# Performance work log

Measured on AMD Instinct MI355X. Metric: run time of the kernel, lower is better.

## Reference

```python
import jax, jax.numpy as jnp
import numpy as np

HEADS = 8
EPS = 1e-6
LN_EPS = 1e-5


def avg_pool(x, k):
    b, c, h, w = x.shape
    return x.reshape(b, c, h // k, k, w // k, k).mean(axis=(3, 5))


def layernorm(x, g, b):
    mu = x.mean(-1, keepdims=True)
    var = x.var(-1, keepdims=True)
    return (x - mu) / jnp.sqrt(var + LN_EPS) * g + b


def pos_embed_2d(h, w, c):
    # original calls build_2d_sincos_position_embedding(w=h, h=w): grid over (h, w), row-major flatten
    gw, gh = jnp.meshgrid(jnp.arange(h, dtype=jnp.float32),
                          jnp.arange(w, dtype=jnp.float32), indexing='ij')
    pd = c // 4
    omega = 1.0 / (10000.0 ** (jnp.arange(pd, dtype=jnp.float32) / pd))
    ow = gw.reshape(-1, 1) * omega  # (h*w, pd)
    oh = gh.reshape(-1, 1) * omega
    return jnp.concatenate([jnp.sin(ow), jnp.cos(ow), jnp.sin(oh), jnp.cos(oh)], axis=1)  # (h*w, c)


def _forward(a3, a4, q_w, q_b, q_ln_g, q_ln_b, k_w, k_b, k_ln_g, k_ln_b,
             v_w, v_b, out_w, out_b, lin1_w, lin1_b, lin2_w, lin2_b,
             n1_g, n1_b, n2_g, n2_b, idx):
    orig_a3 = a3
    if idx == 2:
        a3d = avg_pool(a3, 2)
    else:
        a3d = avg_pool(a3, 4)
        a4 = avg_pool(a4, 2)
    bs, c, h, w = a3d.shape
    L = h * w  # tgt_len == src_len (a3_down and a4 have equal spatial size)
    hd = c // HEADS

    residual = a3d.reshape(bs, c, L).transpose(0, 2, 1)  # (b, L, c)
    x3 = residual
    x4 = a4.reshape(bs, c, L).transpose(0, 2, 1)
    pos = pos_embed_2d(h, w, c)  # (L, c)
    x3 = x3 + pos[None]
    x4 = x4 + pos[None]

    Q = layernorm(x3 @ q_w + q_b, q_ln_g, q_ln_b)
    K = layernorm(x4 @ k_w + k_b, k_ln_g, k_ln_b)
    V = x4 @ v_w + v_b
    Q = jax.nn.relu(Q).reshape(bs, L, HEADS, hd).transpose(0, 2, 1, 3)  # (b,h,L,d)
    K = jax.nn.relu(K).reshape(bs, L, HEADS, hd).transpose(0, 2, 1, 3)
    V = V.reshape(bs, L, HEADS, hd).transpose(0, 2, 1, 3)

    # cosFormer position reweighting: index = pi/2 * (1..m) / m
    m = L
    wi = (np.pi / 2.0) * jnp.arange(1, m + 1, dtype=jnp.float32) / m  # (m,)
    sn = jnp.sin(wi)[None, None, :, None]
    cs = jnp.cos(wi)[None, None, :, None]
    Q_ = jnp.concatenate([Q * sn, Q * cs], axis=-1)  # (b,h,L,2d)
    K_ = jnp.concatenate([K * sn, K * cs], axis=-1)

    KV = jnp.einsum('bhld,bhlm->bhdm', K_, V)                     # (b,h,2d,d)
    Z = 1.0 / jnp.maximum(jnp.einsum('bhld,bhd->bhl', Q_, K_.sum(axis=2)), EPS)
    attn = jnp.einsum('bhld,bhdm->bhlm', Q_, KV) * Z[..., None]   # (b,h,L,d)
    attn = attn.transpose(0, 2, 1, 3).reshape(bs, L, c)

    out = attn @ out_w + out_b
    out = layernorm(out, n1_g, n1_b)     # normalize_before=False -> norm1 applied
    out = residual + out                 # dropout=0
    res2 = out
    out = jax.nn.gelu(out @ lin1_w + lin1_b, approximate=False) @ lin2_w + lin2_b
    out = layernorm(out, n2_g, n2_b)
    out = res2 + out

    a3sa = out.transpose(0, 2, 1).reshape(bs, c, h, w)
    a3sa = jax.image.resize(a3sa, orig_a3.shape, method='bilinear')  # align_corners=False
    return a3sa * orig_a3


def setup_inputs() -> dict:
    key = jax.random.key(0)
    ks = jax.random.split(key, 10)
    B, C = 16, 256
    C4 = 4 * C

    def w(k, shp):
        return jax.random.normal(k, shp, dtype=jnp.float32) * 0.02

    return {
        'a3': jax.random.normal(ks[0], (B, C, 128, 128), dtype=jnp.float32),
        'a4': jax.random.normal(ks[1], (B, C, 64, 64), dtype=jnp.float32),
        'q_w': w(ks[2], (C, C)), 'q_b': jnp.zeros((C,), jnp.float32),
        'q_ln_g': jnp.ones((C,), jnp.float32), 'q_ln_b': jnp.zeros((C,), jnp.float32),
        'k_w': w(ks[3], (C, C)), 'k_b': jnp.zeros((C,), jnp.float32),
        'k_ln_g': jnp.ones((C,), jnp.float32), 'k_ln_b': jnp.zeros((C,), jnp.float32),
        'v_w': w(ks[4], (C, C)), 'v_b': jnp.zeros((C,), jnp.float32),
        'out_w': w(ks[5], (C, C)), 'out_b': jnp.zeros((C,), jnp.float32),
        'lin1_w': w(ks[6], (C, C4)), 'lin1_b': jnp.zeros((C4,), jnp.float32),
        'lin2_w': w(ks[7], (C4, C)), 'lin2_b': jnp.zeros((C,), jnp.float32),
        'n1_g': jnp.ones((C,), jnp.float32), 'n1_b': jnp.zeros((C,), jnp.float32),
        'n2_g': jnp.ones((C,), jnp.float32), 'n2_b': jnp.zeros((C,), jnp.float32),
        'idx': 2,
    }


def reference(a3, a4, q_w, q_b, q_ln_g, q_ln_b, k_w, k_b, k_ln_g, k_ln_b,
              v_w, v_b, out_w, out_b, lin1_w, lin1_b, lin2_w, lin2_b,
              n1_g, n1_b, n2_g, n2_b, idx):
    return _forward(a3, a4, q_w, q_b, q_ln_g, q_ln_b, k_w, k_b, k_ln_g, k_ln_b,
                    v_w, v_b, out_w, out_b, lin1_w, lin1_b, lin2_w, lin2_b,
                    n1_g, n1_b, n2_g, n2_b, idx)
```

## Files before the change

kernel.cpp:

```cpp
#include <hip/hip_runtime.h>
#include <hip/hip_bf16.h>
#include <math.h>

#define HEADS 8
#define LL 4096
#define CDIM 256
#define BATCH 16
#define NROWS (BATCH*LL)

typedef __attribute__((ext_vector_type(8))) __bf16 bf16x8;
typedef __attribute__((ext_vector_type(4))) __bf16 bf16x4;
typedef __attribute__((ext_vector_type(4))) float f32x4;

__device__ inline float b2f(ushort u) {
    union { unsigned u; float f; } v; v.u = ((unsigned)u) << 16; return v.f;
}
__device__ inline ushort f2b(float f) {
    union { float f; unsigned u; } v; v.f = f;
    unsigned r = (v.u + 0x7FFF + ((v.u >> 16) & 1)) >> 16;
    return (ushort)r;
}
__device__ inline void gload16(const void* g, void* l) {
    __builtin_amdgcn_global_load_lds(
        (const __attribute__((address_space(1))) unsigned int*)g,
        (__attribute__((address_space(3))) unsigned int*)l, 16, 0, 0);
}
__device__ inline float fast_gelu(float v) {
    float u = 0.7978845608028654f * v * (1.0f + 0.044715f * v * v);
    float e = exp2f(u * 2.885390081777927f);
    float t = 1.0f - 2.0f / (e + 1.0f);
    return 0.5f * v * (1.0f + t);
}

__global__ __launch_bounds__(256) void prep_kernel(
    float* __restrict__ pos, float* __restrict__ snc,
    const float* __restrict__ q_w, const float* __restrict__ k_w,
    const float* __restrict__ v_w, const float* __restrict__ o_w,
    const float* __restrict__ w1, const float* __restrict__ w2,
    ushort* __restrict__ wqT, ushort* __restrict__ wkT,
    ushort* __restrict__ wvT, ushort* __restrict__ woT,
    ushort* __restrict__ w1T, ushort* __restrict__ w2T,
    float* __restrict__ ksglob)
{
    __shared__ float t[32][33];
    int bid = blockIdx.x;
    int tid = threadIdx.x;
    if (bid == 1792) {
        for (int i = tid; i < BATCH * 2 * 256; i += 256) ksglob[i] = 0.0f;
        return;
    }
    if (bid < 1024) {
        int c = tid;
        int k = c & 63;
        float omega = expf(-(float)k * (9.210340371976184f / 64.0f));
        #pragma unroll
        for (int i = 0; i < 4; ++i) {
            int l = bid * 4 + i;
            int y = l >> 6, x = l & 63;
            float coord = (c < 128) ? (float)y : (float)x;
            float ang = coord * omega;
            float val = ((c & 127) < 64) ? sinf(ang) : cosf(ang);
            pos[l * CDIM + c] = val;
            if (c < 2) {
                float wi = 1.5707963267948966f * (float)(l + 1) / (float)LL;
                snc[l * 2 + c] = (c == 0) ? sinf(wi) : cosf(wi);
            }
        }
        return;
    }
    int id = bid - 1024;
    const float* W; ushort* Wt; int K, N, kb, nb;
    if (id < 64)       { W = q_w; Wt = wqT; K = 256;  N = 256;  kb = (id & 7) * 32;  nb = (id >> 3) * 32; }
    else if (id < 128) { id -= 64;  W = k_w; Wt = wkT; K = 256;  N = 256;  kb = (id & 7) * 32;  nb = (id >> 3) * 32; }
    else if (id < 192) { id -= 128; W = v_w; Wt = wvT; K = 256;  N = 256;  kb = (id & 7) * 32;  nb = (id >> 3) * 32; }
    else if (id < 256) { id -= 192; W = o_w; Wt = woT; K = 256;  N = 256;  kb = (id & 7) * 32;  nb = (id >> 3) * 32; }
    else if (id < 512) { id -= 256; W = w1;  Wt = w1T; K = 256;  N = 1024; kb = (id & 7) * 32;  nb = (id >> 3) * 32; }
    else               { id -= 512; W = w2;  Wt = w2T; K = 1024; N = 256;  kb = (id & 31) * 32; nb = (id >> 5) * 32; }
    int x = tid & 31, y = tid >> 5;
    #pragma unroll
    for (int i = 0; i < 4; ++i)
        t[y + i * 8][x] = W[(size_t)(kb + y + i * 8) * N + nb + x];
    __syncthreads();
    #pragma unroll
    for (int i = 0; i < 4; ++i) {
        int n = y + i * 8;
        Wt[(size_t)(nb + n) * K + kb + x] = f2b(t[x][n]);
    }
}

__global__ __launch_bounds__(256) void pool_x4_kernel(
    const float* __restrict__ a3, const float* __restrict__ a4,
    ushort* __restrict__ residual, ushort* __restrict__ x3b,
    ushort* __restrict__ x4b, const float* __restrict__ pos)
{
    __shared__ float raw[64][128];
    __shared__ float pooled[64][65];
    int tid = threadIdx.x;
    int ct = blockIdx.y;
    if (blockIdx.z < 16) {
        int i = blockIdx.x, b = blockIdx.z;
        #pragma unroll
        for (int it = 0; it < 8; ++it) {
            int lin = (it * 256 + tid) * 4;
            int x = lin & 127;
            int cc = lin >> 7;
            size_t base = ((size_t)(b * 256 + ct * 64 + cc) * 128 + 2 * i) * 128 + x;
            float4 v0 = *(const float4*)&a3[base];
            float4 v1 = *(const float4*)&a3[base + 128];
            float4 s = make_float4(v0.x + v1.x, v0.y + v1.y, v0.z + v1.z, v0.w + v1.w);
            *(float4*)&raw[cc][x] = s;
        }
        __syncthreads();
        #pragma unroll
        for (int it = 0; it < 16; ++it) {
            int idx = it * 256 + tid;
            int j = idx & 63, cc = idx >> 6;
            pooled[cc][j] = 0.25f * (raw[cc][2 * j] + raw[cc][2 * j + 1]);
        }
        __syncthreads();
        #pragma unroll
        for (int it = 0; it < 16; ++it) {
            int cc = tid & 63;
            int jj = (tid >> 6) + it * 4;
            float val = pooled[cc][jj];
            int l = i * 64 + jj;
            int c = ct * 64 + cc;
            size_t o = (size_t)(b * LL + l) * CDIM + c;
            residual[o] = f2b(val);
            x3b[o] = f2b(val + pos[l * CDIM + c]);
        }
    } else {
        int y = blockIdx.x, b = blockIdx.z - 16;
        #pragma unroll
        for (int it = 0; it < 16; ++it) {
            int idx = it * 256 + tid;
            int x = idx & 63, cc = idx >> 6;
            pooled[cc][x] = a4[((size_t)(b * 256 + ct * 64 + cc) * 64 + y) * 64 + x];
        }
        __syncthreads();
        #pragma unroll
        for (int it = 0; it < 16; ++it) {
            int cc = tid & 63;
            int xx = (tid >> 6) + it * 4;
            int l = y * 64 + xx, c = ct * 64 + cc;
            x4b[(size_t)(b * LL + l) * CDIM + c] = f2b(pooled[cc][xx] + pos[l * CDIM + c]);
        }
    }
}

template<bool DO_LN, bool DO_RELU, bool DO_RES>
__global__ __launch_bounds__(512, 4) void gemm_mfma(
    const ushort* __restrict__ A, const ushort* __restrict__ Wt,
    const float* __restrict__ bias, const float* __restrict__ gam_,
    const float* __restrict__ bet_, const ushort* __restrict__ res,
    ushort* __restrict__ outb)
{
    __shared__ ushort As[2][128 * 32];
    __shared__ ushort Bs[2][256 * 32];
    __shared__ float redS[128][4];
    __shared__ float redQ[128][4];
    __shared__ float2 mustd[128];

    const int tid = threadIdx.x;
    const int lane = tid & 63;
    const int wv = tid >> 6;
    const int wr = wv >> 2;
    const int wc = wv & 3;
    const int wvu = __builtin_amdgcn_readfirstlane(wv);
    const int row0 = blockIdx.x * 128;

    const int sr = tid >> 2;
    const int sg = (tid & 3) ^ ((sr >> 1) & 3);
    const ushort* aSrc = A + (size_t)(row0 + sr) * 256 + sg * 8;
    const ushort* bSrc0 = Wt + (size_t)sr * 256 + sg * 8;
    const ushort* bSrc1 = Wt + (size_t)(128 + sr) * 256 + sg * 8;

    const int frSlot = (lane >> 4) ^ (((lane & 15) >> 1) & 3);

    f32x4 acc[4][4] = {};
    gload16(aSrc, (char*)&As[0][0] + wvu * 1024);
    gload16(bSrc0, (char*)&Bs[0][0] + wvu * 1024);
    gload16(bSrc1, (char*)&Bs[0][0] + 8192 + wvu * 1024);
    __syncthreads();

    int cur = 0;
    for (int t = 0; t < 8; ++t) {
        if (t < 7) {
            gload16(aSrc + (t + 1) * 32, (char*)&As[cur ^ 1][0] + wvu * 1024);
            gload16(bSrc0 + (t + 1) * 32, (char*)&Bs[cur ^ 1][0] + wvu * 1024);
            gload16(bSrc1 + (t + 1) * 32, (char*)&Bs[cur ^ 1][0] + 8192 + wvu * 1024);
        }
        bf16x8 af[4], bfr[4];
        #pragma unroll
        for (int f = 0; f < 4; ++f) {
            int r = wr * 64 + f * 16 + (lane & 15);
            af[f] = *(const bf16x8*)&As[cur][r * 32 + frSlot * 8];
            int c = wc * 64 + f * 16 + (lane & 15);
            bfr[f] = *(const bf16x8*)&Bs[cur][c * 32 + frSlot * 8];
        }
        __builtin_amdgcn_s_setprio(1);
        #pragma unroll
        for (int fi = 0; fi < 4; ++fi)
            #pragma unroll
            for (int fj = 0; fj < 4; ++fj)
                acc[fi][fj] = __builtin_amdgcn_mfma_f32_16x16x32_bf16(
                    af[fi], bfr[fj], acc[fi][fj], 0, 0, 0);
        __builtin_amdgcn_s_setprio(0);
        __syncthreads();
        cur ^= 1;
    }

    const int cl = lane & 15;
    const int rg = lane >> 4;
    float bia[4], gmv[4], btv[4];
    #pragma unroll
    for (int fj = 0; fj < 4; ++fj) {
        int col = wc * 64 + fj * 16 + cl;
        bia[fj] = bias[col];
        if constexpr (DO_LN) { gmv[fj] = gam_[col]; btv[fj] = bet_[col]; }
    }
    #pragma unroll
    for (int fi = 0; fi < 4; ++fi)
        #pragma unroll
        for (int fj = 0; fj < 4; ++fj)
            #pragma unroll
            for (int j = 0; j < 4; ++j)
                acc[fi][fj][j] += bia[fj];

    if constexpr (DO_LN) {
        #pragma unroll
        for (int fi = 0; fi < 4; ++fi)
            #pragma unroll
            for (int j = 0; j < 4; ++j) {
                float s = acc[fi][0][j] + acc[fi][1][j] + acc[fi][2][j] + acc[fi][3][j];
                float q = acc[fi][0][j] * acc[fi][0][j] + acc[fi][1][j] * acc[fi][1][j]
                        + acc[fi][2][j] * acc[fi][2][j] + acc[fi][3][j] * acc[fi][3][j];
                #pragma unroll
                for (int m = 1; m <= 8; m <<= 1) {
                    s += __shfl_xor(s, m, 64);
                    q += __shfl_xor(q, m, 64);
                }
                if (cl == 0) {
                    int tr = wr * 64 + fi * 16 + rg * 4 + j;
                    redS[tr][wc] = s; redQ[tr][wc] = q;
                }
            }
        __syncthreads();
        if (tid < 128) {
            float s = redS[tid][0] + redS[tid][1] + redS[tid][2] + redS[tid][3];
            float q = redQ[tid][0] + redQ[tid][1] + redQ[tid][2] + redQ[tid][3];
            float mu = s * (1.0f / 256.0f);
            float var = q * (1.0f / 256.0f) - mu * mu;
            mustd[tid] = make_float2(mu, rsqrtf(var + 1e-5f));
        }
        __syncthreads();
        #pragma unroll
        for (int fi = 0; fi < 4; ++fi)
            #pragma unroll
            for (int j = 0; j < 4; ++j) {
                float2 ms = mustd[wr * 64 + fi * 16 + rg * 4 + j];
                #pragma unroll
                for (int fj = 0; fj < 4; ++fj)
                    acc[fi][fj][j] = (acc[fi][fj][j] - ms.x) * ms.y * gmv[fj] + btv[fj];
            }
    }
    if constexpr (DO_RELU) {
        #pragma unroll
        for (int fi = 0; fi < 4; ++fi)
            #pragma unroll
            for (int fj = 0; fj < 4; ++fj)
                #pragma unroll
                for (int j = 0; j < 4; ++j)
                    acc[fi][fj][j] = fmaxf(acc[fi][fj][j], 0.0f);
    }
    #pragma unroll
    for (int fi = 0; fi < 4; ++fi)
        #pragma unroll
        for (int j = 0; j < 4; ++j) {
            size_t row = row0 + wr * 64 + fi * 16 + rg * 4 + j;
            size_t rbase = row * 256 + wc * 64 + cl;
            #pragma unroll
            for (int fj = 0; fj < 4; ++fj) {
                float v = acc[fi][fj][j];
                if constexpr (DO_RES) v += b2f(res[rbase + fj * 16]);
                outb[rbase + fj * 16] = f2b(v);
            }
        }
}

__global__ __launch_bounds__(512, 2) void gemm_kv(
    const ushort* __restrict__ A, const ushort* __restrict__ wkT,
    const ushort* __restrict__ wvT, const float* __restrict__ k_b,
    const float* __restrict__ k_g, const float* __restrict__ k_beta,
    const float* __restrict__ v_b, const float* __restrict__ snc,
    float* __restrict__ ksglob, ushort* __restrict__ Kb, ushort* __restrict__ Vb)
{
    __shared__ ushort As[2][128 * 32];
    __shared__ ushort BsK[2][256 * 32];
    __shared__ ushort BsV[2][256 * 32];
    float*  redS  = (float*)&As[0][0];
    float*  redQ  = redS + 512;
    float2* mustd = (float2*)(redQ + 512);

    const int tid = threadIdx.x;
    const int lane = tid & 63;
    const int wv = tid >> 6;
    const int wr = wv >> 2;
    const int wc = wv & 3;
    const int wvu = __builtin_amdgcn_readfirstlane(wv);
    const int row0 = blockIdx.x * 128;

    const int sr = tid >> 2;
    const int sg = (tid & 3) ^ ((sr >> 1) & 3);
    const ushort* aSrc = A + (size_t)(row0 + sr) * 256 + sg * 8;
    const ushort* bkSrc0 = wkT + (size_t)sr * 256 + sg * 8;
    const ushort* bkSrc1 = wkT + (size_t)(128 + sr) * 256 + sg * 8;
    const ushort* bvSrc0 = wvT + (size_t)sr * 256 + sg * 8;
    const ushort* bvSrc1 = wvT + (size_t)(128 + sr) * 256 + sg * 8;

    const int frSlot = (lane >> 4) ^ (((lane & 15) >> 1) & 3);

    f32x4 accK[4][4] = {};
    f32x4 accV[4][4] = {};
    gload16(aSrc, (char*)&As[0][0] + wvu * 1024);
    gload16(bkSrc0, (char*)&BsK[0][0] + wvu * 1024);
    gload16(bkSrc1, (char*)&BsK[0][0] + 8192 + wvu * 1024);
    gload16(bvSrc0, (char*)&BsV[0][0] + wvu * 1024);
    gload16(bvSrc1, (char*)&BsV[0][0] + 8192 + wvu * 1024);
    __syncthreads();

    int cur = 0;
    for (int t = 0; t < 8; ++t) {
        if (t < 7) {
            gload16(aSrc + (t + 1) * 32, (char*)&As[cur ^ 1][0] + wvu * 1024);
            gload16(bkSrc0 + (t + 1) * 32, (char*)&BsK[cur ^ 1][0] + wvu * 1024);
            gload16(bkSrc1 + (t + 1) * 32, (char*)&BsK[cur ^ 1][0] + 8192 + wvu * 1024);
            gload16(bvSrc0 + (t + 1) * 32, (char*)&BsV[cur ^ 1][0] + wvu * 1024);
            gload16(bvSrc1 + (t + 1) * 32, (char*)&BsV[cur ^ 1][0] + 8192 + wvu * 1024);
        }
        bf16x8 af[4], bk[4], bv[4];
        #pragma unroll
        for (int f = 0; f < 4; ++f) {
            int r = wr * 64 + f * 16 + (lane & 15);
            af[f] = *(const bf16x8*)&As[cur][r * 32 + frSlot * 8];
            int c = wc * 64 + f * 16 + (lane & 15);
            bk[f] = *(const bf16x8*)&BsK[cur][c * 32 + frSlot * 8];
            bv[f] = *(const bf16x8*)&BsV[cur][c * 32 + frSlot * 8];
        }
        __builtin_amdgcn_s_setprio(1);
        #pragma unroll
        for (int fi = 0; fi < 4; ++fi)
            #pragma unroll
            for (int fj = 0; fj < 4; ++fj) {
                accK[fi][fj] = __builtin_amdgcn_mfma_f32_16x16x32_bf16(
                    af[fi], bk[fj], accK[fi][fj], 0, 0, 0);
                accV[fi][fj] = __builtin_amdgcn_mfma_f32_16x16x32_bf16(
                    af[fi], bv[fj], accV[fi][fj], 0, 0, 0);
            }
        __builtin_amdgcn_s_setprio(0);
        __syncthreads();
        cur ^= 1;
    }

    const int cl = lane & 15;
    const int rg = lane >> 4;
    #pragma unroll
    for (int fj = 0; fj < 4; ++fj) {
        float bv_ = v_b[wc * 64 + fj * 16 + cl];
        #pragma unroll
        for (int fi = 0; fi < 4; ++fi)
            #pragma unroll
            for (int j = 0; j < 4; ++j)
                accV[fi][fj][j] += bv_;
    }
    #pragma unroll
    for (int fi = 0; fi < 4; ++fi)
        #pragma unroll
        for (int j = 0; j < 4; ++j) {
            size_t rbase = (size_t)(row0 + wr * 64 + fi * 16 + rg * 4 + j) * 256 + wc * 64 + cl;
            #pragma unroll
            for (int fj = 0; fj < 4; ++fj)
                Vb[rbase + fj * 16] = f2b(accV[fi][fj][j]);
        }
    float bia[4], gmv[4], btv[4];
    #pragma unroll
    for (int fj = 0; fj < 4; ++fj) {
        int col = wc * 64 + fj * 16 + cl;
        bia[fj] = k_b[col]; gmv[fj] = k_g[col]; btv[fj] = k_beta[col];
    }
    #pragma unroll
    for (int fi = 0; fi < 4; ++fi)
        #pragma unroll
        for (int fj = 0; fj < 4; ++fj)
            #pragma unroll
            for (int j = 0; j < 4; ++j)
                accK[fi][fj][j] += bia[fj];
    #pragma unroll
    for (int fi = 0; fi < 4; ++fi)
        #pragma unroll
        for (int j = 0; j < 4; ++j) {
            float s = accK[fi][0][j] + accK[fi][1][j] + accK[fi][2][j] + accK[fi][3][j];
            float q = accK[fi][0][j] * accK[fi][0][j] + accK[fi][1][j] * accK[fi][1][j]
                    + accK[fi][2][j] * accK[fi][2][j] + accK[fi][3][j] * accK[fi][3][j];
            #pragma unroll
            for (int m = 1; m <= 8; m <<= 1) {
                s += __shfl_xor(s, m, 64);
                q += __shfl_xor(q, m, 64);
            }
            if (cl == 0) {
                int tr = wr * 64 + fi * 16 + rg * 4 + j;
                redS[tr * 4 + wc] = s; redQ[tr * 4 + wc] = q;
            }
        }
    __syncthreads();
    if (tid < 128) {
        float s = redS[tid * 4] + redS[tid * 4 + 1] + redS[tid * 4 + 2] + redS[tid * 4 + 3];
        float q = redQ[tid * 4] + redQ[tid * 4 + 1] + redQ[tid * 4 + 2] + redQ[tid * 4 + 3];
        float mu = s * (1.0f / 256.0f);
        float var = q * (1.0f / 256.0f) - mu * mu;
        mustd[tid] = make_float2(mu, rsqrtf(var + 1e-5f));
    }
    __syncthreads();
    float kss[4] = {}, ksc[4] = {};
    #pragma unroll
    for (int fi = 0; fi < 4; ++fi)
        #pragma unroll
        for (int j = 0; j < 4; ++j) {
            int rloc = wr * 64 + fi * 16 + rg * 4 + j;
            float2 ms = mustd[rloc];
            int l = (row0 + rloc) & (LL - 1);
            float sn = snc[l * 2], cs = snc[l * 2 + 1];
            size_t rbase = (size_t)(row0 + rloc) * 256 + wc * 64 + cl;
            #pragma unroll
            for (int fj = 0; fj < 4; ++fj) {
                float v = (accK[fi][fj][j] - ms.x) * ms.y * gmv[fj] + btv[fj];
                v = fmaxf(v, 0.0f);
                Kb[rbase + fj * 16] = f2b(v);
                kss[fj] += sn * v;
                ksc[fj] += cs * v;
            }
        }
    int b = row0 >> 12;
    #pragma unroll
    for (int fj = 0; fj < 4; ++fj) {
        float s = kss[fj], c = ksc[fj];
        s += __shfl_xor(s, 16, 64); s += __shfl_xor(s, 32, 64);
        c += __shfl_xor(c, 16, 64); c += __shfl_xor(c, 32, 64);
        if (rg == 0) {
            int col = wc * 64 + fj * 16 + cl;
            atomicAdd(&ksglob[((size_t)b * 2 + 0) * 256 + col], s);
            atomicAdd(&ksglob[((size_t)b * 2 + 1) * 256 + col], c);
        }
    }
}

__global__ __launch_bounds__(256, 2) void mlp_fused(
    const ushort* __restrict__ res2, const ushort* __restrict__ w1T,
    const ushort* __restrict__ w2T, const float* __restrict__ b1,
    const float* __restrict__ b2, const float* __restrict__ gam_,
    const float* __restrict__ bet_, ushort* __restrict__ outb)
{
    __shared__ ushort As[2][64 * 32];
    __shared__ ushort Bs[2][256 * 32];
    __shared__ ushort h1c[8 * 64 * 36];
    __shared__ float redS[64][4];
    __shared__ float redQ[64][4];
    __shared__ float2 mustd[64];

    const int tid = threadIdx.x;
    const int lane = tid & 63;
    const int wv = tid >> 6;
    const int wvu = __builtin_amdgcn_readfirstlane(wv);
    const int row0 = blockIdx.x * 64;
    const int sr = tid >> 2;
    const int sg = (tid & 3) ^ ((sr >> 1) & 3);
    const ushort* aSrc = res2 + (size_t)(row0 + sr) * 256 + sg * 8;
    const int frSlot = (lane >> 4) ^ (((lane & 15) >> 1) & 3);
    const int cl = lane & 15;
    const int rg = lane >> 4;

    f32x4 acc2[4][4] = {};
    gload16(aSrc, (char*)&As[0][0] + wvu * 1024);
    #pragma unroll
    for (int j = 0; j < 4; ++j)
        gload16(w1T + (size_t)(j * 64 + sr) * 256 + sg * 8,
                (char*)&Bs[0][0] + j * 4096 + wvu * 1024);
    __syncthreads();
    int cur = 0;

    for (int c = 0; c < 4; ++c) {
        const ushort* b1Src = w1T + (size_t)(c * 256 + sr) * 256 + sg * 8;
        const ushort* b2Src = w2T + (size_t)sr * 1024 + c * 256 + sg * 8;
        f32x4 acc1[4][4] = {};
        for (int t = 0; t < 8; ++t) {
            if (t < 7) {
                gload16(aSrc + (t + 1) * 32, (char*)&As[cur ^ 1][0] + wvu * 1024);
                #pragma unroll
                for (int j = 0; j < 4; ++j)
                    gload16(b1Src + j * 64 * 256 + (t + 1) * 32,
                            (char*)&Bs[cur ^ 1][0] + j * 4096 + wvu * 1024);
            } else {
                gload16(aSrc, (char*)&As[cur ^ 1][0] + wvu * 1024);
                #pragma unroll
                for (int j = 0; j < 4; ++j)
                    gload16(b2Src + (size_t)j * 64 * 1024,
                            (char*)&Bs[cur ^ 1][0] + j * 4096 + wvu * 1024);
            }
            bf16x8 af[4], bfr[4];
            #pragma unroll
            for (int f = 0; f < 4; ++f) {
                int r = f * 16 + (lane & 15);
                af[f] = *(const bf16x8*)&As[cur][r * 32 + frSlot * 8];
                int cc2 = wv * 64 + f * 16 + (lane & 15);
                bfr[f] = *(const bf16x8*)&Bs[cur][cc2 * 32 + frSlot * 8];
            }
            __builtin_amdgcn_s_setprio(1);
            #pragma unroll
            for (int fi = 0; fi < 4; ++fi)
                #pragma unroll
                for (int fj = 0; fj < 4; ++fj)
                    acc1[fi][fj] = __builtin_amdgcn_mfma_f32_16x16x32_bf16(
                        af[fi], bfr[fj], acc1[fi][fj], 0, 0, 0);
            __builtin_amdgcn_s_setprio(0);
            __syncthreads();
            cur ^= 1;
        }
        float bia1[4];
        #pragma unroll
        for (int fj = 0; fj < 4; ++fj)
            bia1[fj] = b1[c * 256 + wv * 64 + fj * 16 + cl];
        #pragma unroll
        for (int fi = 0; fi < 4; ++fi)
            #pragma unroll
            for (int fj = 0; fj < 4; ++fj) {
                int tch = wv * 2 + (fj >> 1);
                int kk_local = (fj & 1) * 16 + cl;
                #pragma unroll
                for (int j = 0; j < 4; ++j) {
                    float v = acc1[fi][fj][j] + bia1[fj];
                    float g = fast_gelu(v);
                    int row = fi * 16 + rg * 4 + j;
                    h1c[tch * 2304 + row * 36 + kk_local] = f2b(g);
                }
            }
        __syncthreads();
        for (int t = 0; t < 8; ++t) {
            if (t < 7) {
                #pragma unroll
                for (int j = 0; j < 4; ++j)
                    gload16(b2Src + (size_t)j * 64 * 1024 + (t + 1) * 32,
                            (char*)&Bs[cur ^ 1][0] + j * 4096 + wvu * 1024);
            } else {
                int cn = (c < 3) ? c + 1 : 3;
                #pragma unroll
                for (int j = 0; j < 4; ++j)
                    gload16(w1T + (size_t)(cn * 256 + j * 64 + sr) * 256 + sg * 8,
                            (char*)&Bs[cur ^ 1][0] + j * 4096 + wvu * 1024);
            }
            bf16x8 af[4], bfr[4];
            #pragma unroll
            for (int f = 0; f < 4; ++f) {
                int r = f * 16 + (lane & 15);
                int ho = t * 2304 + r * 36 + (lane >> 4) * 8;
                bf16x4 lo = *(const bf16x4*)&h1c[ho];
                bf16x4 hi = *(const bf16x4*)&h1c[ho + 4];
                bf16x8 a_;
                a_[0] = lo[0]; a_[1] = lo[1]; a_[2] = lo[2]; a_[3] = lo[3];
                a_[4] = hi[0]; a_[5] = hi[1]; a_[6] = hi[2]; a_[7] = hi[3];
                af[f] = a_;
                int cc2 = wv * 64 + f * 16 + (lane & 15);
                bfr[f] = *(const bf16x8*)&Bs[cur][cc2 * 32 + frSlot * 8];
            }
            __builtin_amdgcn_s_setprio(1);
            #pragma unroll
            for (int fi = 0; fi < 4; ++fi)
                #pragma unroll
                for (int fj = 0; fj < 4; ++fj)
                    acc2[fi][fj] = __builtin_amdgcn_mfma_f32_16x16x32_bf16(
                        af[fi], bfr[fj], acc2[fi][fj], 0, 0, 0);
            __builtin_amdgcn_s_setprio(0);
            __syncthreads();
            cur ^= 1;
        }
    }
    float bia[4], gmv[4], btv[4];
    #pragma unroll
    for (int fj = 0; fj < 4; ++fj) {
        int col = wv * 64 + fj * 16 + cl;
        bia[fj] = b2[col];
        gmv[fj] = gam_[col];
        btv[fj] = bet_[col];
    }
    #pragma unroll
    for (int fi = 0; fi < 4; ++fi)
        #pragma unroll
        for (int fj = 0; fj < 4; ++fj)
            #pragma unroll
            for (int j = 0; j < 4; ++j)
                acc2[fi][fj][j] += bia[fj];
    #pragma unroll
    for (int fi = 0; fi < 4; ++fi)
        #pragma unroll
        for (int j = 0; j < 4; ++j) {
            float s = acc2[fi][0][j] + acc2[fi][1][j] + acc2[fi][2][j] + acc2[fi][3][j];
            float q = acc2[fi][0][j] * acc2[fi][0][j] + acc2[fi][1][j] * acc2[fi][1][j]
                    + acc2[fi][2][j] * acc2[fi][2][j] + acc2[fi][3][j] * acc2[fi][3][j];
            #pragma unroll
            for (int m = 1; m <= 8; m <<= 1) {
                s += __shfl_xor(s, m, 64);
                q += __shfl_xor(q, m, 64);
            }
            if (cl == 0) { redS[fi * 16 + rg * 4 + j][wv] = s; redQ[fi * 16 + rg * 4 + j][wv] = q; }
        }
    __syncthreads();
    if (tid < 64) {
        float s = redS[tid][0] + redS[tid][1] + redS[tid][2] + redS[tid][3];
        float q = redQ[tid][0] + redQ[tid][1] + redQ[tid][2] + redQ[tid][3];
        float mu = s * (1.0f / 256.0f);
        float var = q * (1.0f / 256.0f) - mu * mu;
        mustd[tid] = make_float2(mu, rsqrtf(var + 1e-5f));
    }
    __syncthreads();
    #pragma unroll
    for (int fi = 0; fi < 4; ++fi)
        #pragma unroll
        for (int j = 0; j < 4; ++j) {
            float2 ms = mustd[fi * 16 + rg * 4 + j];
            size_t row = row0 + fi * 16 + rg * 4 + j;
            size_t rbase = row * 256 + wv * 64 + cl;
            #pragma unroll
            for (int fj = 0; fj < 4; ++fj) {
                float v = (acc2[fi][fj][j] - ms.x) * ms.y * gmv[fj] + btv[fj];
                v += b2f(res2[rbase + fj * 16]);
                outb[rbase + fj * 16] = f2b(v);
            }
        }
}

__global__ __launch_bounds__(256) void kv_kernel(
    const ushort* __restrict__ Kmat, const ushort* __restrict__ Vmat,
    const float* __restrict__ snc, float* __restrict__ kvpart)
{
    __shared__ float Kt[64][36];
    __shared__ float Vt[64][36];
    __shared__ float sns[64], css[64];
    int chunk = blockIdx.x;
    int bh = blockIdx.y;
    int b = bh >> 3, h = bh & 7;
    int tid = threadIdx.x;
    int m = tid & 31;
    int d0 = (tid >> 5) * 4;
    float accs[4] = {}, accc[4] = {};
    int l0chunk = chunk * 512;
    int lrow = tid >> 2;
    int lcol = (tid & 3) * 8;
    for (int sub = 0; sub < 8; ++sub) {
        int l0 = l0chunk + sub * 64;
        {
            size_t gbase = (size_t)(b * LL + l0 + lrow) * CDIM + h * 32 + lcol;
            uint4 kr = *(const uint4*)&Kmat[gbase];
            uint4 vr = *(const uint4*)&Vmat[gbase];
            float* kd = &Kt[lrow][lcol];
            float* vd = &Vt[lrow][lcol];
            kd[0] = b2f((ushort)(kr.x & 0xffff)); kd[1] = b2f((ushort)(kr.x >> 16));
            kd[2] = b2f((ushort)(kr.y & 0xffff)); kd[3] = b2f((ushort)(kr.y >> 16));
            kd[4] = b2f((ushort)(kr.z & 0xffff)); kd[5] = b2f((ushort)(kr.z >> 16));
            kd[6] = b2f((ushort)(kr.w & 0xffff)); kd[7] = b2f((ushort)(kr.w >> 16));
            vd[0] = b2f((ushort)(vr.x & 0xffff)); vd[1] = b2f((ushort)(vr.x >> 16));
            vd[2] = b2f((ushort)(vr.y & 0xffff)); vd[3] = b2f((ushort)(vr.y >> 16));
            vd[4] = b2f((ushort)(vr.z & 0xffff)); vd[5] = b2f((ushort)(vr.z >> 16));
            vd[6] = b2f((ushort)(vr.w & 0xffff)); vd[7] = b2f((ushort)(vr.w >> 16));
        }
        if (tid < 64) { sns[tid] = snc[(l0 + tid) * 2]; css[tid] = snc[(l0 + tid) * 2 + 1]; }
        __syncthreads();
        #pragma unroll 4
        for (int lt = 0; lt < 64; ++lt) {
            float v = Vt[lt][m];
            float vs = v * sns[lt];
            float vc = v * css[lt];
            float4 kd4 = *(const float4*)&Kt[lt][d0];
            accs[0] += kd4.x * vs; accc[0] += kd4.x * vc;
            accs[1] += kd4.y * vs; accc[1] += kd4.y * vc;
            accs[2] += kd4.z * vs; accc[2] += kd4.z * vc;
            accs[3] += kd4.w * vs; accc[3] += kd4.w * vc;
        }
        __syncthreads();
    }
    size_t base = (size_t)(bh * 8 + chunk) * 2048;
    #pragma unroll
    for (int i2 = 0; i2 < 4; ++i2) {
        kvpart[base + (d0 + i2) * 32 + m] = accs[i2];
        kvpart[base + 1024 + (d0 + i2) * 32 + m] = accc[i2];
    }
}

__global__ __launch_bounds__(256) void kvred_kernel(
    const float* __restrict__ kvpart, const float* __restrict__ ksglob,
    ushort* __restrict__ Bimg)
{
    int bh = blockIdx.x;
    int b = bh >> 3, h = bh & 7;
    int tid = threadIdx.x;
    for (int e = tid; e < 2560; e += 256) {
        int n = e >> 5;
        int k = e & 31;
        int t = n >> 4, col = n & 15;
        float v = 0.0f;
        if (t < 4) {
            int off = (t >= 2 ? 1024 : 0) + k * 32 + (t & 1) * 16 + col;
            #pragma unroll
            for (int ch = 0; ch < 8; ++ch)
                v += kvpart[(size_t)(bh * 8 + ch) * 2048 + off];
        } else if (col < 2) {
            v = ksglob[((size_t)b * 2 + col) * 256 + h * 32 + k];
        }
        ushort hi = f2b(v);
        ushort lo = f2b(v - b2f(hi));
        Bimg[(size_t)bh * 5120 + n * 32 + k] = hi;
        Bimg[(size_t)bh * 5120 + (80 + n) * 32 + k] = lo;
    }
}

__global__ __launch_bounds__(256, 2) void attn_mfma(
    const ushort* __restrict__ Qmat, const ushort* __restrict__ Bimg,
    const float* __restrict__ snc, ushort* __restrict__ attnOut)
{
    __shared__ ushort Bs[5120];
    int ltile = blockIdx.x, h = blockIdx.y, b = blockIdx.z;
    int bh = b * 8 + h;
    int tid = threadIdx.x;
    int lane = tid & 63;
    int wv = tid >> 6;

    for (int e = tid; e < 640; e += 256)
        *(uint4*)&Bs[e * 8] = *(const uint4*)&Bimg[(size_t)bh * 5120 + e * 8];
    __syncthreads();

    bf16x8 bfr[10];
    #pragma unroll
    for (int tt = 0; tt < 10; ++tt) {
        int row = (tt < 5 ? tt * 16 : 80 + (tt - 5) * 16) + (lane & 15);
        bfr[tt] = *(const bf16x8*)&Bs[row * 32 + (lane >> 4) * 8];
    }
    int lbase = ltile * 256 + wv * 64;
    bf16x8 af[4];
    #pragma unroll
    for (int fi = 0; fi < 4; ++fi) {
        int l = lbase + fi * 16 + (lane & 15);
        af[fi] = *(const bf16x8*)&Qmat[(size_t)(b * LL + l) * CDIM + h * 32 + (lane >> 4) * 8];
    }
    f32x4 acc[4][5] = {};
    __builtin_amdgcn_s_setprio(1);
    #pragma unroll
    for (int fi = 0; fi < 4; ++fi)
        #pragma unroll
        for (int t = 0; t < 5; ++t) {
            acc[fi][t] = __builtin_amdgcn_mfma_f32_16x16x32_bf16(af[fi], bfr[t], acc[fi][t], 0, 0, 0);
            acc[fi][t] = __builtin_amdgcn_mfma_f32_16x16x32_bf16(af[fi], bfr[t + 5], acc[fi][t], 0, 0, 0);
        }
    __builtin_amdgcn_s_setprio(0);

    int zlane = lane & 48;
    int cl = lane & 15;
    #pragma unroll
    for (int fi = 0; fi < 4; ++fi) {
        #pragma unroll
        for (int j = 0; j < 4; ++j) {
            float zraw = acc[fi][4][j];
            float zs = __shfl(zraw, zlane, 64);
            float zc = __shfl(zraw, zlane | 1, 64);
            int l = lbase + fi * 16 + ((lane >> 4) & 3) * 4 + j;
            float sn = snc[l * 2], cs = snc[l * 2 + 1];
            float den = sn * zs + cs * zc;
            float Z = 1.0f / fmaxf(den, 1e-6f);
            float v0 = (sn * acc[fi][0][j] + cs * acc[fi][2][j]) * Z;
            float v1 = (sn * acc[fi][1][j] + cs * acc[fi][3][j]) * Z;
            size_t ob = (size_t)(b * LL + l) * CDIM + h * 32 + cl;
            attnOut[ob] = f2b(v0);
            attnOut[ob + 16] = f2b(v1);
        }
    }
}

__global__ __launch_bounds__(256) void resize_mul_kernel(
    const ushort* __restrict__ ffeat, const float* __restrict__ a3, float* __restrict__ out)
{
    __shared__ float ft[3][64][65];
    int k = blockIdx.x, ct = blockIdx.y, b = blockIdx.z;
    int tid = threadIdx.x;
    #pragma unroll
    for (int it = 0; it < 6; ++it) {
        int e = it * 256 + tid;
        int cg = e & 7;
        int xs = (e >> 3) & 63;
        int ys = e >> 9;
        int ysrc = min(max(k - 1 + ys, 0), 63);
        uint4 raw = *(const uint4*)&ffeat[(size_t)(b * LL + ysrc * 64 + xs) * CDIM + ct * 64 + cg * 8];
        float* dst = &ft[ys][cg * 8][xs];
        dst[0]   = b2f((ushort)(raw.x & 0xffff)); dst[65]  = b2f((ushort)(raw.x >> 16));
        dst[130] = b2f((ushort)(raw.y & 0xffff)); dst[195] = b2f((ushort)(raw.y >> 16));
        dst[260] = b2f((ushort)(raw.z & 0xffff)); dst[325] = b2f((ushort)(raw.z >> 16));
        dst[390] = b2f((ushort)(raw.w & 0xffff)); dst[455] = b2f((ushort)(raw.w >> 16));
    }
    __syncthreads();
    int x = tid & 127;
    int half = tid >> 7;
    int y = 2 * k + half;
    int ysA, ysB; float wyA, wyB;
    if (half == 0) { ysA = 0; ysB = 1; wyA = 0.25f; wyB = 0.75f; }
    else           { ysA = 1; ysB = 2; wyA = 0.75f; wyB = 0.25f; }
    int x0; float wx1;
    if ((x & 1) == 0) { x0 = x / 2 - 1; wx1 = 0.75f; }
    else              { x0 = x / 2;     wx1 = 0.25f; }
    int x0c = max(x0, 0);
    int x1c = min(x0 + 1, 63);
    float wx0 = 1.0f - wx1;
    for (int cc = 0; cc < 64; ++cc) {
        float rA = wx0 * ft[ysA][cc][x0c] + wx1 * ft[ysA][cc][x1c];
        float rB = wx0 * ft[ysB][cc][x0c] + wx1 * ft[ysB][cc][x1c];
        float val = wyA * rA + wyB * rB;
        size_t oidx = ((size_t)(b * 256 + ct * 64 + cc) * 128 + y) * 128 + x;
        out[oidx] = val * a3[oidx];
    }
}

extern "C" void kernel_launch(void* const* d_in, const int* in_sizes, int n_in,
                              void* d_out, int out_size, void* d_ws, size_t ws_size,
                              hipStream_t stream)
{
    const float* a3     = (const float*)d_in[0];
    const float* a4     = (const float*)d_in[1];
    const float* q_w    = (const float*)d_in[2];
    const float* q_b    = (const float*)d_in[3];
    const float* q_ln_g = (const float*)d_in[4];
    const float* q_ln_b = (const float*)d_in[5];
    const float* k_w    = (const float*)d_in[6];
    const float* k_b    = (const float*)d_in[7];
    const float* k_ln_g = (const float*)d_in[8];
    const float* k_ln_b = (const float*)d_in[9];
    const float* v_w    = (const float*)d_in[10];
    const float* v_b    = (const float*)d_in[11];
    const float* out_w  = (const float*)d_in[12];
    const float* out_b  = (const float*)d_in[13];
    const float* lin1_w = (const float*)d_in[14];
    const float* lin1_b = (const float*)d_in[15];
    const float* lin2_w = (const float*)d_in[16];
    const float* lin2_b = (const float*)d_in[17];
    const float* n1_g   = (const float*)d_in[18];
    const float* n1_b   = (const float*)d_in[19];
    const float* n2_g   = (const float*)d_in[20];
    const float* n2_b   = (const float*)d_in[21];
    float* out = (float*)d_out;
    char* base = (char*)d_ws;

    const size_t MiB = 1024 * 1024;
    float*  pos      = (float*)(base);
    float*  snc      = (float*)(base + 4 * MiB);
    ushort* wqT      = (ushort*)(base + 4 * MiB + 64 * 1024);
    ushort* wkT      = wqT + 256 * 256;
    ushort* wvT      = wkT + 256 * 256;
    ushort* woT      = wvT + 256 * 256;
    ushort* w1T      = woT + 256 * 256;
    ushort* w2T      = w1T + 1024 * 256;
    ushort* residual = (ushort*)(base + 6 * MiB);
    ushort* x3b      = (ushort*)(base + 38 * MiB);
    ushort* x4b      = (ushort*)(base + 70 * MiB);
    ushort* Qb       = (ushort*)(base + 102 * MiB);
    ushort* Kb       = (ushort*)(base + 134 * MiB);
    ushort* Vb       = (ushort*)(base + 166 * MiB);
    float*  kvp      = (float*)(base + 198 * MiB);
    float*  ksglob   = (float*)(base + 206 * MiB);
    ushort* Bimg     = (ushort*)(base + 207 * MiB);
    ushort* attnb    = x3b;
    ushort* res2b    = x4b;
    ushort* ffeat    = residual;

    prep_kernel<<<1793, 256, 0, stream>>>(pos, snc, q_w, k_w, v_w, out_w, lin1_w, lin2_w,
                                          wqT, wkT, wvT, woT, w1T, w2T, ksglob);
    pool_x4_kernel<<<dim3(64, 4, 32), 256, 0, stream>>>(a3, a4, residual, x3b, x4b, pos);

    gemm_mfma<true, true, false><<<NROWS / 128, 512, 0, stream>>>(
        x3b, wqT, q_b, q_ln_g, q_ln_b, nullptr, Qb);
    gemm_kv<<<NROWS / 128, 512, 0, stream>>>(
        x4b, wkT, wvT, k_b, k_ln_g, k_ln_b, v_b, snc, ksglob, Kb, Vb);

    kv_kernel<<<dim3(8, 128), 256, 0, stream>>>(Kb, Vb, snc, kvp);
    kvred_kernel<<<128, 256, 0, stream>>>(kvp, ksglob, Bimg);
    attn_mfma<<<dim3(16, 8, 16), 256, 0, stream>>>(Qb, Bimg, snc, attnb);

    gemm_mfma<true, false, true><<<NROWS / 128, 512, 0, stream>>>(
        attnb, woT, out_b, n1_g, n1_b, residual, res2b);
    mlp_fused<<<NROWS / 64, 256, 0, stream>>>(
        res2b, w1T, w2T, lin1_b, lin2_b, n2_g, n2_b, ffeat);

    resize_mul_kernel<<<dim3(64, 4, 16), 256, 0, stream>>>(ffeat, a3, out);
}
```

Measured before the change: 529.7 us.

## Merge prep and pooling kernels, fold kv reduction into attention kernel

Prep and pooling now run as a single kernel that computes the positional embedding inline instead of reading a precomputed table. Weight transposes and the snc/ksglob init move to extra grid slices, removing one launch and the 4 MiB pos buffer round trip. The kv reduction kernel is removed: each attention block reduces kvpart partials and builds its bf16 hi/lo B image directly in shared memory. The cost is redundant reduction work, repeated 16 times per (b,h) across l-tiles, plus extra transcendental math in the pooling path. Ordering is risky: gemm_kv accumulates into ksglob, which is now zeroed by one block of the same kernel that also transposes the weights, so correctness relies on the kernel boundary.

Measured after the change: 566.1 us. +6.9%, slower.

```diff
diff --git a/kernel.cpp b/kernel.cpp
--- a/kernel.cpp
+++ b/kernel.cpp
@@ -31,74 +31,35 @@
     float t = 1.0f - 2.0f / (e + 1.0f);
     return 0.5f * v * (1.0f + t);
 }
-
-__global__ __launch_bounds__(256) void prep_kernel(
-    float* __restrict__ pos, float* __restrict__ snc,
+__device__ inline float posval(int l, int c) {
+    int k = c & 63;
+    float omega = expf(-(float)k * (9.210340371976184f / 64.0f));
+    float coord = (c < 128) ? (float)(l >> 6) : (float)(l & 63);
+    float ang = coord * omega;
+    return ((c & 127) < 64) ? sinf(ang) : cosf(ang);
+}
+
+__global__ __launch_bounds__(256) void mega_prep_kernel(
+    const float* __restrict__ a3, const float* __restrict__ a4,
+    ushort* __restrict__ residual, ushort* __restrict__ x3b,
+    ushort* __restrict__ x4b,
     const float* __restrict__ q_w, const float* __restrict__ k_w,
     const float* __restrict__ v_w, const float* __restrict__ o_w,
     const float* __restrict__ w1, const float* __restrict__ w2,
     ushort* __restrict__ wqT, ushort* __restrict__ wkT,
     ushort* __restrict__ wvT, ushort* __restrict__ woT,
     ushort* __restrict__ w1T, ushort* __restrict__ w2T,
-    float* __restrict__ ksglob)
-{
-    __shared__ float t[32][33];
-    int bid = blockIdx.x;
-    int tid = threadIdx.x;
-    if (bid == 1792) {
-        for (int i = tid; i < BATCH * 2 * 256; i += 256) ksglob[i] = 0.0f;
-        return;
-    }
-    if (bid < 1024) {
-        int c = tid;
-        int k = c & 63;
-        float omega = expf(-(float)k * (9.210340371976184f / 64.0f));
-        #pragma unroll
-        for (int i = 0; i < 4; ++i) {
-            int l = bid * 4 + i;
-            int y = l >> 6, x = l & 63;
-            float coord = (c < 128) ? (float)y : (float)x;
-            float ang = coord * omega;
-            float val = ((c & 127) < 64) ? sinf(ang) : cosf(ang);
-            pos[l * CDIM + c] = val;
-            if (c < 2) {
-                float wi = 1.5707963267948966f * (float)(l + 1) / (float)LL;
-                snc[l * 2 + c] = (c == 0) ? sinf(wi) : cosf(wi);
-            }
-        }
-        return;
-    }
-    int id = bid - 1024;
-    const float* W; ushort* Wt; int K, N, kb, nb;
-    if (id < 64)       { W = q_w; Wt = wqT; K = 256;  N = 256;  kb = (id & 7) * 32;  nb = (id >> 3) * 32; }
-    else if (id < 128) { id -= 64;  W = k_w; Wt = wkT; K = 256;  N = 256;  kb = (id & 7) * 32;  nb = (id >> 3) * 32; }
-    else if (id < 192) { id -= 128; W = v_w; Wt = wvT; K = 256;  N = 256;  kb = (id & 7) * 32;  nb = (id >> 3) * 32; }
-    else if (id < 256) { id -= 192; W = o_w; Wt = woT; K = 256;  N = 256;  kb = (id & 7) * 32;  nb = (id >> 3) * 32; }
-    else if (id < 512) { id -= 256; W = w1;  Wt = w1T; K = 256;  N = 1024; kb = (id & 7) * 32;  nb = (id >> 3) * 32; }
-    else               { id -= 512; W = w2;  Wt = w2T; K = 1024; N = 256;  kb = (id & 31) * 32; nb = (id >> 5) * 32; }
-    int x = tid & 31, y = tid >> 5;
-    #pragma unroll
-    for (int i = 0; i < 4; ++i)
-        t[y + i * 8][x] = W[(size_t)(kb + y + i * 8) * N + nb + x];
-    __syncthreads();
-    #pragma unroll
-    for (int i = 0; i < 4; ++i) {
-        int n = y + i * 8;
-        Wt[(size_t)(nb + n) * K + kb + x] = f2b(t[x][n]);
-    }
-}
-
-__global__ __launch_bounds__(256) void pool_x4_kernel(
-    const float* __restrict__ a3, const float* __restrict__ a4,
-    ushort* __restrict__ residual, ushort* __restrict__ x3b,
-    ushort* __restrict__ x4b, const float* __restrict__ pos)
+    float* __restrict__ snc, float* __restrict__ ksglob)
 {
     __shared__ float raw[64][128];
     __shared__ float pooled[64][65];
+    __shared__ float t[32][33];
     int tid = threadIdx.x;
     int ct = blockIdx.y;
-    if (blockIdx.z < 16) {
-        int i = blockIdx.x, b = blockIdx.z;
+    int z = blockIdx.z;
+
+    if (z < 16) {
+        int i = blockIdx.x, b = z;
         #pragma unroll
         for (int it = 0; it < 8; ++it) {
             int lin = (it * 256 + tid) * 4;
@@ -127,10 +88,12 @@
             int c = ct * 64 + cc;
             size_t o = (size_t)(b * LL + l) * CDIM + c;
             residual[o] = f2b(val);
-            x3b[o] = f2b(val + pos[l * CDIM + c]);
-        }
-    } else {
-        int y = blockIdx.x, b = blockIdx.z - 16;
+            x3b[o] = f2b(val + posval(l, c));
+        }
+        return;
+    }
+    if (z < 32) {
+        int y = blockIdx.x, b = z - 16;
         #pragma unroll
         for (int it = 0; it < 16; ++it) {
             int idx = it * 256 + tid;
@@ -143,8 +106,38 @@
             int cc = tid & 63;
             int xx = (tid >> 6) + it * 4;
             int l = y * 64 + xx, c = ct * 64 + cc;
-            x4b[(size_t)(b * LL + l) * CDIM + c] = f2b(pooled[cc][xx] + pos[l * CDIM + c]);
-        }
+            x4b[(size_t)(b * LL + l) * CDIM + c] = f2b(pooled[cc][xx] + posval(l, c));
+        }
+        return;
+    }
+    if (z == 35) {
+        if (blockIdx.x != 0 || blockIdx.y != 0) return;
+        for (int i = 0; i < 16; ++i) {
+            int l = i * 256 + tid;
+            float wi = 1.5707963267948966f * (float)(l + 1) / (float)LL;
+            snc[l * 2] = sinf(wi);
+            snc[l * 2 + 1] = cosf(wi);
+        }
+        for (int i = tid; i < BATCH * 2 * 256; i += 256) ksglob[i] = 0.0f;
+        return;
+    }
+    int id = (z - 32) * 256 + blockIdx.y * 64 + blockIdx.x;
+    const float* W; ushort* Wt; int K, N, kb, nb;
+    if (id < 64)       { W = q_w; Wt = wqT; K = 256;  N = 256;  kb = (id & 7) * 32;  nb = (id >> 3) * 32; }
+    else if (id < 128) { id -= 64;  W = k_w; Wt = wkT; K = 256;  N = 256;  kb = (id & 7) * 32;  nb = (id >> 3) * 32; }
+    else if (id < 192) { id -= 128; W = v_w; Wt = wvT; K = 256;  N = 256;  kb = (id & 7) * 32;  nb = (id >> 3) * 32; }
+    else if (id < 256) { id -= 192; W = o_w; Wt = woT; K = 256;  N = 256;  kb = (id & 7) * 32;  nb = (id >> 3) * 32; }
+    else if (id < 512) { id -= 256; W = w1;  Wt = w1T; K = 256;  N = 1024; kb = (id & 7) * 32;  nb = (id >> 3) * 32; }
+    else               { id -= 512; W = w2;  Wt = w2T; K = 1024; N = 256;  kb = (id & 31) * 32; nb = (id >> 5) * 32; }
+    int x = tid & 31, y = tid >> 5;
+    #pragma unroll
+    for (int i = 0; i < 4; ++i)
+        t[y + i * 8][x] = W[(size_t)(kb + y + i * 8) * N + nb + x];
+    __syncthreads();
+    #pragma unroll
+    for (int i = 0; i < 4; ++i) {
+        int n = y + i * 8;
+        Wt[(size_t)(nb + n) * K + kb + x] = f2b(t[x][n]);
     }
 }
 
@@ -694,13 +687,18 @@
     }
 }
 
-__global__ __launch_bounds__(256) void kvred_kernel(
-    const float* __restrict__ kvpart, const float* __restrict__ ksglob,
-    ushort* __restrict__ Bimg)
+__global__ __launch_bounds__(256, 2) void attn_mfma(
+    const ushort* __restrict__ Qmat, const float* __restrict__ kvpart,
+    const float* __restrict__ ksglob, const float* __restrict__ snc,
+    ushort* __restrict__ attnOut)
 {
-    int bh = blockIdx.x;
-    int b = bh >> 3, h = bh & 7;
+    __shared__ ushort Bs[5120];
+    int ltile = blockIdx.x, h = blockIdx.y, b = blockIdx.z;
+    int bh = b * 8 + h;
     int tid = threadIdx.x;
+    int lane = tid & 63;
+    int wv = tid >> 6;
+
     for (int e = tid; e < 2560; e += 256) {
         int n = e >> 5;
         int k = e & 31;
@@ -716,24 +714,9 @@
         }
         ushort hi = f2b(v);
         ushort lo = f2b(v - b2f(hi));
-        Bimg[(size_t)bh * 5120 + n * 32 + k] = hi;
-        Bimg[(size_t)bh * 5120 + (80 + n) * 32 + k] = lo;
-    }
-}
-
-__global__ __launch_bounds__(256, 2) void attn_mfma(
-    const ushort* __restrict__ Qmat, const ushort* __restrict__ Bimg,
-    const float* __restrict__ snc, ushort* __restrict__ attnOut)
-{
-    __shared__ ushort Bs[5120];
-    int ltile = blockIdx.x, h = blockIdx.y, b = blockIdx.z;
-    int bh = b * 8 + h;
-    int tid = threadIdx.x;
-    int lane = tid & 63;
-    int wv = tid >> 6;
-
-    for (int e = tid; e < 640; e += 256)
-        *(uint4*)&Bs[e * 8] = *(const uint4*)&Bimg[(size_t)bh * 5120 + e * 8];
+        Bs[n * 32 + k] = hi;
+        Bs[(80 + n) * 32 + k] = lo;
+    }
     __syncthreads();
 
     bf16x8 bfr[10];
@@ -854,7 +837,6 @@
     char* base = (char*)d_ws;
 
     const size_t MiB = 1024 * 1024;
-    float*  pos      = (float*)(base);
     float*  snc      = (float*)(base + 4 * MiB);
     ushort* wqT      = (ushort*)(base + 4 * MiB + 64 * 1024);
     ushort* wkT      = wqT + 256 * 256;
@@ -870,14 +852,14 @@
     ushort* Vb       = (ushort*)(base + 166 * MiB);
     float*  kvp      = (float*)(base + 198 * MiB);
     float*  ksglob   = (float*)(base + 206 * MiB);
-    ushort* Bimg     = (ushort*)(base + 207 * MiB);
     ushort* attnb    = x3b;
     ushort* res2b    = x4b;
     ushort* ffeat    = residual;
 
-    prep_kernel<<<1793, 256, 0, stream>>>(pos, snc, q_w, k_w, v_w, out_w, lin1_w, lin2_w,
-                                          wqT, wkT, wvT, woT, w1T, w2T, ksglob);
-    pool_x4_kernel<<<dim3(64, 4, 32), 256, 0, stream>>>(a3, a4, residual, x3b, x4b, pos);
+    mega_prep_kernel<<<dim3(64, 4, 36), 256, 0, stream>>>(
+        a3, a4, residual, x3b, x4b,
+        q_w, k_w, v_w, out_w, lin1_w, lin2_w,
+        wqT, wkT, wvT, woT, w1T, w2T, snc, ksglob);
 
     gemm_mfma<true, true, false><<<NROWS / 128, 512, 0, stream>>>(
         x3b, wqT, q_b, q_ln_g, q_ln_b, nullptr, Qb);
@@ -885,8 +867,7 @@
         x4b, wkT, wvT, k_b, k_ln_g, k_ln_b, v_b, snc, ksglob, Kb, Vb);
 
     kv_kernel<<<dim3(8, 128), 256, 0, stream>>>(Kb, Vb, snc, kvp);
-    kvred_kernel<<<128, 256, 0, stream>>>(kvp, ksglob, Bimg);
-    attn_mfma<<<dim3(16, 8, 16), 256, 0, stream>>>(Qb, Bimg, snc, attnb);
+    attn_mfma<<<dim3(16, 8, 16), 256, 0, stream>>>(Qb, kvp, ksglob, snc, attnb);
 
     gemm_mfma<true, false, true><<<NROWS / 128, 512, 0, stream>>>(
         attnb, woT, out_b, n1_g, n1_b, residual, res2b);
```
